# Kernel optimization log

Measured on AMD Instinct MI355X. Metric: run time of the kernel, lower is better.

## Reference

```python
import jax, jax.numpy as jnp
import numpy as np

K = 32        # neighbors per anchor (cfg.k)
LN_EPS = 1e-6 # flax LayerNorm default


def _layer_norm(x, g, b):
    mu = jnp.mean(x, axis=-1, keepdims=True)
    var = jnp.var(x, axis=-1, keepdims=True)
    return (x - mu) * jax.lax.rsqrt(var + LN_EPS) * g + b


def setup_inputs() -> dict:
    key = jax.random.key(0)
    ks = jax.random.split(key, 8)
    b, n, m, c = 4, 8192, 2048, 64
    feats, hidden = 128, 64  # cfg.features, cfg.features // 2
    cin = 3 + c              # delta_coord (3) concat neighbor feats (c)
    feat = jax.random.normal(ks[0], (b, n, c), jnp.float32)
    coord = jax.random.uniform(ks[1], (b, n, 3), jnp.float32)
    anchor_feat = jax.random.normal(ks[2], (b, m, c), jnp.float32)
    anchor_coord = jax.random.uniform(ks[3], (b, m, 3), jnp.float32)
    W1 = jax.random.normal(ks[4], (cin, hidden), jnp.float32) / np.sqrt(cin).astype(np.float32)
    b1 = jnp.zeros((hidden,), jnp.float32)
    g1 = jnp.ones((hidden,), jnp.float32)
    be1 = jnp.zeros((hidden,), jnp.float32)
    W2 = jax.random.normal(ks[5], (hidden, feats), jnp.float32) / np.sqrt(hidden).astype(np.float32)
    b2 = jnp.zeros((feats,), jnp.float32)
    g2 = jnp.ones((feats,), jnp.float32)
    be2 = jnp.zeros((feats,), jnp.float32)
    return dict(feat=feat, coord=coord, anchor_feat=anchor_feat,
                anchor_coord=anchor_coord, W1=W1, b1=b1, g1=g1, be1=be1,
                W2=W2, b2=b2, g2=g2, be2=be2)


def reference(feat, coord, anchor_feat, anchor_coord,
              W1, b1, g1, be1, W2, b2, g2, be2):
    # --- kNN: squared distances [b, m, n], take K smallest ---
    d2 = (jnp.sum(anchor_coord ** 2, axis=-1)[..., None]
          - 2.0 * jnp.einsum('bmd,bnd->bmn', anchor_coord, coord)
          + jnp.sum(coord ** 2, axis=-1)[:, None, :])
    _, idx = jax.lax.top_k(-d2, K)  # idx: [b, m, K]

    gather = jax.vmap(lambda arr, i: arr[i])  # batch_lookup
    k_feat = gather(feat, idx) - anchor_feat[..., None, :]   # [b,m,K,c] (anchor_feat_offset)
    k_coord = gather(coord, idx)                             # [b,m,K,3]

    delta = k_coord - anchor_coord[..., None, :]             # [b,m,K,3]
    norms = jnp.linalg.norm(delta, axis=-1, keepdims=True)   # [b,m,K,1]
    delta = delta / jnp.max(norms, axis=(-1, -2, -3), keepdims=True)  # per-batch max norm

    x = jnp.concatenate([delta, k_feat], axis=-1)            # [b,m,K,3+c]
    # GroupMLP: Dense -> LN -> relu, Dense -> LN -> relu, max pool over K
    x = jax.nn.relu(_layer_norm(x @ W1 + b1, g1, be1))
    x = jax.nn.relu(_layer_norm(x @ W2 + b2, g2, be2))
    return jnp.max(x, axis=-2)                               # [b, m, features]
```

## Files before the change

kernel.cpp:

```cpp
#include <hip/hip_runtime.h>
#include <math.h>

#define BB 4
#define NN 8192
#define MM 2048
#define CC 64
#define KNB 32
#define CIN 67
#define H1 64
#define H2 128
#define XP 36
#define AB 4
#define KT 512
#define PJ 16

__global__ void init_kernel(int* maxnorm) {
    if (threadIdx.x < BB) maxnorm[threadIdx.x] = 0;
}

__global__ __launch_bounds__(256) void coord4_kernel(const float* __restrict__ coord,
                                                     float4* __restrict__ c4) {
    const int t = blockIdx.x * 256 + threadIdx.x;
    if (t < BB * NN) {
        float cx = coord[t * 3 + 0], cy = coord[t * 3 + 1], cz = coord[t * 3 + 2];
        float c2 = __fadd_rn(__fadd_rn(__fmul_rn(cx, cx), __fmul_rn(cy, cy)), __fmul_rn(cz, cz));
        float4 q; q.x = cx; q.y = cy; q.z = cz; q.w = c2;
        c4[t] = q;
    }
}

__global__ __launch_bounds__(KT, 8) void knn_kernel(
    const float4* __restrict__ c4buf, const float* __restrict__ anchor_coord,
    int* __restrict__ idxbuf, int* __restrict__ maxnorm)
{
    __shared__ unsigned hist[2][4][256];
    __shared__ unsigned wmax[2][8];
    __shared__ unsigned wtot[2][4];
    __shared__ unsigned bc[2][2];
    __shared__ unsigned nsel[2];
    __shared__ int      selcell[2];
    __shared__ int      sel_s[2][KNB];

    const int a0 = blockIdx.x * 2;
    const int b  = a0 >> 11;
    const int mi = a0 & (MM - 1);
    const int tid = threadIdx.x;
    const int w = tid >> 6, lane = tid & 63;

    const float axA = anchor_coord[(b * MM + mi) * 3 + 0];
    const float ayA = anchor_coord[(b * MM + mi) * 3 + 1];
    const float azA = anchor_coord[(b * MM + mi) * 3 + 2];
    const float a2A = __fadd_rn(__fadd_rn(__fmul_rn(axA, axA), __fmul_rn(ayA, ayA)), __fmul_rn(azA, azA));
    const float axB = anchor_coord[(b * MM + mi + 1) * 3 + 0];
    const float ayB = anchor_coord[(b * MM + mi + 1) * 3 + 1];
    const float azB = anchor_coord[(b * MM + mi + 1) * 3 + 2];
    const float a2B = __fadd_rn(__fadd_rn(__fmul_rn(axB, axB), __fmul_rn(ayB, ayB)), __fmul_rn(azB, azB));

    const float4* c4b = c4buf + (size_t)b * NN;

    unsigned kregA[PJ], kregB[PJ];
    unsigned tminA = 0xFFFFFFFFu, tminB = 0xFFFFFFFFu;
    #pragma unroll
    for (int j = 0; j < PJ; j++) {
        const int i = tid + KT * j;
        const float4 cq = c4b[i];
        float dtA = __fadd_rn(__fadd_rn(__fmul_rn(axA, cq.x), __fmul_rn(ayA, cq.y)), __fmul_rn(azA, cq.z));
        float d2A = __fadd_rn(__fsub_rn(a2A, __fmul_rn(2.0f, dtA)), cq.w);
        unsigned ubA = __float_as_uint(d2A);
        ubA ^= (unsigned)((int)ubA >> 31) | 0x80000000u;
        kregA[j] = ubA;
        tminA = tminA < ubA ? tminA : ubA;
        float dtB = __fadd_rn(__fadd_rn(__fmul_rn(axB, cq.x), __fmul_rn(ayB, cq.y)), __fmul_rn(azB, cq.z));
        float d2B = __fadd_rn(__fsub_rn(a2B, __fmul_rn(2.0f, dtB)), cq.w);
        unsigned ubB = __float_as_uint(d2B);
        ubB ^= (unsigned)((int)ubB >> 31) | 0x80000000u;
        kregB[j] = ubB;
        tminB = tminB < ubB ? tminB : ubB;
    }

    unsigned umA = tminA, umB = tminB;
    umA = max(umA, (unsigned)__shfl_xor((int)umA, 1));
    umA = max(umA, (unsigned)__shfl_xor((int)umA, 2));
    umB = max(umB, (unsigned)__shfl_xor((int)umB, 1));
    umB = max(umB, (unsigned)__shfl_xor((int)umB, 2));
    if (lane == 0) { wmax[0][w] = umA; wmax[1][w] = umB; }
    if (tid == 0) { nsel[0] = 0; nsel[1] = 0; }
    __syncthreads();
    unsigned UA = wmax[0][0], UB = wmax[1][0];
    #pragma unroll
    for (int q = 1; q < 8; q++) { UA = max(UA, wmax[0][q]); UB = max(UB, wmax[1][q]); }

    unsigned prefA = 0, prefB = 0, pmask = 0;
    unsigned kA = KNB, kB = KNB;
    const int hc = w >> 1;

    #pragma unroll
    for (int pass = 0; pass < 4; pass++) {
        const int sh = 24 - 8 * pass;
        unsigned* hf = &hist[0][0][0];
        #pragma unroll
        for (int q = 0; q < 4; q++) hf[tid + KT * q] = 0;
        __syncthreads();
        if (pass == 0) {
            #pragma unroll
            for (int j = 0; j < PJ; j++) {
                if (kregA[j] <= UA) atomicAdd(&hist[0][hc][kregA[j] >> 24], 1u);
                if (kregB[j] <= UB) atomicAdd(&hist[1][hc][kregB[j] >> 24], 1u);
            }
        } else {
            #pragma unroll
            for (int j = 0; j < PJ; j++) {
                if ((kregA[j] & pmask) == prefA) atomicAdd(&hist[0][hc][(kregA[j] >> sh) & 0xFFu], 1u);
                if ((kregB[j] & pmask) == prefB) atomicAdd(&hist[1][hc][(kregB[j] >> sh) & 0xFFu], 1u);
            }
        }
        __syncthreads();
        if (tid < 256) {
            const unsigned hA = hist[0][0][tid] + hist[0][1][tid] + hist[0][2][tid] + hist[0][3][tid];
            const unsigned hB = hist[1][0][tid] + hist[1][1][tid] + hist[1][2][tid] + hist[1][3][tid];
            unsigned vA = hA, vB = hB;
            #pragma unroll
            for (int d = 1; d < 64; d <<= 1) {
                unsigned tA = __shfl_up(vA, d);
                unsigned tB = __shfl_up(vB, d);
                if (lane >= d) { vA += tA; vB += tB; }
            }
            if (lane == 63) { wtot[0][w] = vA; wtot[1][w] = vB; }
        }
        __syncthreads();
        if (tid < 256) {
            const unsigned hA = hist[0][0][tid] + hist[0][1][tid] + hist[0][2][tid] + hist[0][3][tid];
            const unsigned hB = hist[1][0][tid] + hist[1][1][tid] + hist[1][2][tid] + hist[1][3][tid];
            unsigned vA = hA, vB = hB;
            #pragma unroll
            for (int d = 1; d < 64; d <<= 1) {
                unsigned tA = __shfl_up(vA, d);
                unsigned tB = __shfl_up(vB, d);
                if (lane >= d) { vA += tA; vB += tB; }
            }
            unsigned offA = 0, offB = 0;
            #pragma unroll
            for (int ww = 0; ww < 3; ww++) if (ww < w) { offA += wtot[0][ww]; offB += wtot[1][ww]; }
            vA += offA; vB += offB;
            const unsigned exclA = vA - hA, exclB = vB - hB;
            if (exclA < kA && kA <= vA) { bc[0][0] = (unsigned)tid; bc[0][1] = kA - exclA; }
            if (exclB < kB && kB <= vB) { bc[1][0] = (unsigned)tid; bc[1][1] = kB - exclB; }
        }
        __syncthreads();
        prefA |= bc[0][0] << sh; kA = bc[0][1];
        prefB |= bc[1][0] << sh; kB = bc[1][1];
        pmask |= 0xFFu << sh;
    }
    const unsigned TA = prefA, TB = prefB;

    unsigned tiemaskA = 0, tiemaskB = 0;
    #pragma unroll
    for (int j = 0; j < PJ; j++) {
        unsigned kkA = kregA[j];
        if (kkA < TA) { unsigned p = atomicAdd(&nsel[0], 1u); sel_s[0][p] = tid + KT * j; }
        else if (kkA == TA) tiemaskA |= 1u << j;
        unsigned kkB = kregB[j];
        if (kkB < TB) { unsigned p = atomicAdd(&nsel[1], 1u); sel_s[1][p] = tid + KT * j; }
        else if (kkB == TB) tiemaskB |= 1u << j;
    }
    __syncthreads();
    {
        const unsigned n_lt = nsel[0];
        const unsigned needed = KNB - n_lt;
        int last = -1;
        for (unsigned r = 0; r < needed; r++) {
            if (tid == 0) selcell[0] = 0x7fffffff;
            __syncthreads();
            unsigned m = tiemaskA;
            while (m) {
                int j = __ffs(m) - 1; m &= m - 1;
                int idx = tid + KT * j;
                if (idx > last) atomicMin(&selcell[0], idx);
            }
            __syncthreads();
            last = selcell[0];
            if (tid == 0) sel_s[0][n_lt + r] = last;
            __syncthreads();
        }
    }
    {
        const unsigned n_lt = nsel[1];
        const unsigned needed = KNB - n_lt;
        int last = -1;
        for (unsigned r = 0; r < needed; r++) {
            if (tid == 0) selcell[1] = 0x7fffffff;
            __syncthreads();
            unsigned m = tiemaskB;
            while (m) {
                int j = __ffs(m) - 1; m &= m - 1;
                int idx = tid + KT * j;
                if (idx > last) atomicMin(&selcell[1], idx);
            }
            __syncthreads();
            last = selcell[1];
            if (tid == 0) sel_s[1][n_lt + r] = last;
            __syncthreads();
        }
    }

    float nrm = 0.0f;
    if (tid < 64) {
        const int a = tid >> 5;
        const int s = tid & 31;
        const int j = sel_s[a][s];
        idxbuf[(size_t)(a0 + a) * KNB + s] = j;
        const float4 cq = c4b[j];
        const float ax = a ? axB : axA, ay = a ? ayB : ayA, az = a ? azB : azA;
        float dx = __fsub_rn(cq.x, ax);
        float dy = __fsub_rn(cq.y, ay);
        float dz = __fsub_rn(cq.z, az);
        nrm = sqrtf(dx * dx + dy * dy + dz * dz);
        #pragma unroll
        for (int off = 32; off; off >>= 1) nrm = fmaxf(nrm, __shfl_xor(nrm, off));
        if (tid == 0) atomicMax(&maxnorm[b], __float_as_int(nrm));
    }
}

__global__ __launch_bounds__(256, 4) void mlp_kernel(
    const float* __restrict__ feat, const float* __restrict__ coord,
    const float* __restrict__ anchor_feat, const float* __restrict__ anchor_coord,
    const float* __restrict__ W1, const float* __restrict__ b1,
    const float* __restrict__ g1, const float* __restrict__ be1,
    const float* __restrict__ W2, const float* __restrict__ b2,
    const float* __restrict__ g2, const float* __restrict__ be2,
    const int* __restrict__ maxnorm, const int* __restrict__ idxbuf,
    float* __restrict__ out)
{
    __shared__ __align__(16) float xst[AB][CIN * XP];
    __shared__ int sel[AB][KNB];

    const int a0g = blockIdx.x * AB;
    const int b   = a0g >> 11;
    const int tid = threadIdx.x;
    const int w = tid >> 6, lane = tid & 63;
    const int g = tid >> 5, c = tid & 31;

    if (tid < AB * KNB) sel[tid >> 5][tid & 31] = idxbuf[(size_t)a0g * KNB + tid];
    __syncthreads();

    const float mn = __int_as_float(maxnorm[b]);

    {
        const int mi = (a0g + w) & (MM - 1);
        const float af = anchor_feat[((size_t)b * MM + mi) * CC + lane];
        #pragma unroll 8
        for (int kk = 0; kk < KNB; kk++) {
            const int nj = sel[w][kk];
            xst[w][(3 + lane) * XP + kk] = feat[((size_t)b * NN + nj) * CC + lane] - af;
        }
    }
    for (int t = tid; t < AB * KNB * 3; t += 256) {
        const int a = t / 96, r = t % 96, k = r / 3, j = r % 3;
        const int mi = (a0g + a) & (MM - 1);
        const int nj = sel[a][k];
        float d = __fsub_rn(coord[((size_t)b * NN + nj) * 3 + j],
                            anchor_coord[((size_t)b * MM + mi) * 3 + j]);
        xst[a][j * XP + k] = __fdiv_rn(d, mn);
    }
    __syncthreads();

    const int ch1 = 2 * c;
    const float b1a = b1[ch1], b1b = b1[ch1 + 1];
    float accA[AB][4], accB[AB][4];
    #pragma unroll
    for (int a = 0; a < AB; a++)
        #pragma unroll
        for (int kk = 0; kk < 4; kk++) { accA[a][kk] = b1a; accB[a][kk] = b1b; }
    #pragma unroll 4
    for (int j = 0; j < CIN; j++) {
        const float2 wv = *(const float2*)&W1[j * H1 + ch1];
        #pragma unroll
        for (int a = 0; a < AB; a++) {
            const float4 xq = *(const float4*)&xst[a][j * XP + 4 * g];
            accA[a][0] = fmaf(xq.x, wv.x, accA[a][0]);  accB[a][0] = fmaf(xq.x, wv.y, accB[a][0]);
            accA[a][1] = fmaf(xq.y, wv.x, accA[a][1]);  accB[a][1] = fmaf(xq.y, wv.y, accB[a][1]);
            accA[a][2] = fmaf(xq.z, wv.x, accA[a][2]);  accB[a][2] = fmaf(xq.z, wv.y, accB[a][2]);
            accA[a][3] = fmaf(xq.w, wv.x, accA[a][3]);  accB[a][3] = fmaf(xq.w, wv.y, accB[a][3]);
        }
    }
    const float g1a = g1[ch1], g1b = g1[ch1 + 1];
    const float be1a = be1[ch1], be1b = be1[ch1 + 1];
    float y1A[AB][4], y1B[AB][4];
    #pragma unroll
    for (int a = 0; a < AB; a++) {
        #pragma unroll
        for (int kk = 0; kk < 4; kk++) {
            float s  = accA[a][kk] + accB[a][kk];
            float s2 = accA[a][kk] * accA[a][kk] + accB[a][kk] * accB[a][kk];
            #pragma unroll
            for (int off = 16; off; off >>= 1) { s += __shfl_xor(s, off); s2 += __shfl_xor(s2, off); }
            float mu  = s  * (1.0f / H1);
            float var = s2 * (1.0f / H1) - mu * mu;
            float r = rsqrtf(var + 1e-6f);
            y1A[a][kk] = fmaxf(fmaf((accA[a][kk] - mu) * r, g1a, be1a), 0.0f);
            y1B[a][kk] = fmaxf(fmaf((accB[a][kk] - mu) * r, g1b, be1b), 0.0f);
        }
    }
    __syncthreads();
    #pragma unroll
    for (int a = 0; a < AB; a++)
        #pragma unroll
        for (int kk = 0; kk < 4; kk++) {
            xst[a][ch1 * XP + 4 * g + kk]       = y1A[a][kk];
            xst[a][(ch1 + 1) * XP + 4 * g + kk] = y1B[a][kk];
        }
    __syncthreads();

    const int ch2 = 4 * c;
    const float4 b2v = *(const float4*)&b2[ch2];
    float a2c[AB][16];
    #pragma unroll
    for (int a = 0; a < AB; a++)
        #pragma unroll
        for (int kk = 0; kk < 4; kk++) {
            a2c[a][0 * 4 + kk] = b2v.x; a2c[a][1 * 4 + kk] = b2v.y;
            a2c[a][2 * 4 + kk] = b2v.z; a2c[a][3 * 4 + kk] = b2v.w;
        }
    #pragma unroll 2
    for (int j = 0; j < H1; j++) {
        const float4 wv = *(const float4*)&W2[j * H2 + ch2];
        #pragma unroll
        for (int a = 0; a < AB; a++) {
            const float4 hq = *(const float4*)&xst[a][j * XP + 4 * g];
            a2c[a][0]  = fmaf(hq.x, wv.x, a2c[a][0]);  a2c[a][1]  = fmaf(hq.y, wv.x, a2c[a][1]);
            a2c[a][2]  = fmaf(hq.z, wv.x, a2c[a][2]);  a2c[a][3]  = fmaf(hq.w, wv.x, a2c[a][3]);
            a2c[a][4]  = fmaf(hq.x, wv.y, a2c[a][4]);  a2c[a][5]  = fmaf(hq.y, wv.y, a2c[a][5]);
            a2c[a][6]  = fmaf(hq.z, wv.y, a2c[a][6]);  a2c[a][7]  = fmaf(hq.w, wv.y, a2c[a][7]);
            a2c[a][8]  = fmaf(hq.x, wv.z, a2c[a][8]);  a2c[a][9]  = fmaf(hq.y, wv.z, a2c[a][9]);
            a2c[a][10] = fmaf(hq.z, wv.z, a2c[a][10]); a2c[a][11] = fmaf(hq.w, wv.z, a2c[a][11]);
            a2c[a][12] = fmaf(hq.x, wv.w, a2c[a][12]); a2c[a][13] = fmaf(hq.y, wv.w, a2c[a][13]);
            a2c[a][14] = fmaf(hq.z, wv.w, a2c[a][14]); a2c[a][15] = fmaf(hq.w, wv.w, a2c[a][15]);
        }
    }
    const float4 g2v  = *(const float4*)&g2[ch2];
    const float4 be2v = *(const float4*)&be2[ch2];
    float mx[AB][4];
    #pragma unroll
    for (int a = 0; a < AB; a++) {
        mx[a][0] = -INFINITY; mx[a][1] = -INFINITY; mx[a][2] = -INFINITY; mx[a][3] = -INFINITY;
        #pragma unroll
        for (int kk = 0; kk < 4; kk++) {
            float v0 = a2c[a][kk], v1 = a2c[a][4 + kk], v2 = a2c[a][8 + kk], v3 = a2c[a][12 + kk];
            float s  = (v0 + v1) + (v2 + v3);
            float s2 = (v0 * v0 + v1 * v1) + (v2 * v2 + v3 * v3);
            #pragma unroll
            for (int off = 16; off; off >>= 1) { s += __shfl_xor(s, off); s2 += __shfl_xor(s2, off); }
            float mu  = s  * (1.0f / H2);
            float var = s2 * (1.0f / H2) - mu * mu;
            float r = rsqrtf(var + 1e-6f);
            mx[a][0] = fmaxf(mx[a][0], fmaxf(fmaf((v0 - mu) * r, g2v.x, be2v.x), 0.0f));
            mx[a][1] = fmaxf(mx[a][1], fmaxf(fmaf((v1 - mu) * r, g2v.y, be2v.y), 0.0f));
            mx[a][2] = fmaxf(mx[a][2], fmaxf(fmaf((v2 - mu) * r, g2v.z, be2v.z), 0.0f));
            mx[a][3] = fmaxf(mx[a][3], fmaxf(fmaf((v3 - mu) * r, g2v.w, be2v.w), 0.0f));
        }
    }
    __syncthreads();
    float* pmaxp = &xst[0][0];
    #pragma unroll
    for (int a = 0; a < AB; a++) {
        float4 q; q.x = mx[a][0]; q.y = mx[a][1]; q.z = mx[a][2]; q.w = mx[a][3];
        *(float4*)&pmaxp[(a * 8 + g) * H2 + ch2] = q;
    }
    __syncthreads();
    #pragma unroll
    for (int t = tid; t < AB * H2; t += 256) {
        const int a = t >> 7, ch = t & 127;
        float vv = pmaxp[(a * 8 + 0) * H2 + ch];
        #pragma unroll
        for (int gg = 1; gg < 8; gg++) vv = fmaxf(vv, pmaxp[(a * 8 + gg) * H2 + ch]);
        out[(size_t)(a0g + a) * H2 + ch] = vv;
    }
}

extern "C" void kernel_launch(void* const* d_in, const int* in_sizes, int n_in,
                              void* d_out, int out_size, void* d_ws, size_t ws_size,
                              hipStream_t stream) {
    const float* feat         = (const float*)d_in[0];
    const float* coord        = (const float*)d_in[1];
    const float* anchor_feat  = (const float*)d_in[2];
    const float* anchor_coord = (const float*)d_in[3];
    const float* W1  = (const float*)d_in[4];
    const float* b1  = (const float*)d_in[5];
    const float* g1  = (const float*)d_in[6];
    const float* be1 = (const float*)d_in[7];
    const float* W2  = (const float*)d_in[8];
    const float* b2  = (const float*)d_in[9];
    const float* g2  = (const float*)d_in[10];
    const float* be2 = (const float*)d_in[11];
    float* out = (float*)d_out;

    int*    maxn   = (int*)d_ws;
    int*    idxbuf = (int*)d_ws + 16;
    float4* c4buf  = (float4*)((int*)d_ws + 16 + BB * MM * KNB);

    init_kernel<<<1, 64, 0, stream>>>(maxn);
    coord4_kernel<<<(BB * NN + 255) / 256, 256, 0, stream>>>(coord, c4buf);
    knn_kernel<<<BB * MM / 2, KT, 0, stream>>>(c4buf, anchor_coord, idxbuf, maxn);
    mlp_kernel<<<BB * MM / AB, 256, 0, stream>>>(feat, coord, anchor_feat, anchor_coord,
                                                 W1, b1, g1, be1, W2, b2, g2, be2,
                                                 maxn, idxbuf, out);
}
```

Baseline: 215.9 us.

## Process four anchors per kNN block to amortize coordinate loads and scans

The kNN kernel now handles four anchors per 512-thread block instead of two. Each coordinate load and each radix-select pass is shared across more anchors, and the scan work is split so all 512 threads take part, each half covering two anchors. The cost is many more live registers (64 keys per thread), with launch bounds lowered from 8 to 4 blocks, so occupancy may drop. Histogram copies per anchor fall from 4 to 2, which raises LDS atomic contention.

```diff
diff --git a/kernel.cpp b/kernel.cpp
--- a/kernel.cpp
+++ b/kernel.cpp
@@ -13,6 +13,7 @@
 #define AB 4
 #define KT 512
 #define PJ 16
+#define KAB 4
 
 __global__ void init_kernel(int* maxnorm) {
     if (threadIdx.x < BB) maxnorm[threadIdx.x] = 0;
@@ -29,19 +30,19 @@
     }
 }
 
-__global__ __launch_bounds__(KT, 8) void knn_kernel(
+__global__ __launch_bounds__(KT, 4) void knn_kernel(
     const float4* __restrict__ c4buf, const float* __restrict__ anchor_coord,
     int* __restrict__ idxbuf, int* __restrict__ maxnorm)
 {
-    __shared__ unsigned hist[2][4][256];
-    __shared__ unsigned wmax[2][8];
-    __shared__ unsigned wtot[2][4];
-    __shared__ unsigned bc[2][2];
-    __shared__ unsigned nsel[2];
-    __shared__ int      selcell[2];
-    __shared__ int      sel_s[2][KNB];
-
-    const int a0 = blockIdx.x * 2;
+    __shared__ unsigned hist[KAB][2][256];
+    __shared__ unsigned wmax[KAB][8];
+    __shared__ unsigned wtot[KAB][4];
+    __shared__ unsigned bc[KAB][2];
+    __shared__ unsigned nsel[KAB];
+    __shared__ int      selcell[KAB];
+    __shared__ int      sel_s[KAB][KNB];
+
+    const int a0 = blockIdx.x * KAB;
     const int b  = a0 >> 11;
     const int mi = a0 & (MM - 1);
     const int tid = threadIdx.x;
@@ -55,11 +56,19 @@
     const float ayB = anchor_coord[(b * MM + mi + 1) * 3 + 1];
     const float azB = anchor_coord[(b * MM + mi + 1) * 3 + 2];
     const float a2B = __fadd_rn(__fadd_rn(__fmul_rn(axB, axB), __fmul_rn(ayB, ayB)), __fmul_rn(azB, azB));
+    const float axC = anchor_coord[(b * MM + mi + 2) * 3 + 0];
+    const float ayC = anchor_coord[(b * MM + mi + 2) * 3 + 1];
+    const float azC = anchor_coord[(b * MM + mi + 2) * 3 + 2];
+    const float a2C = __fadd_rn(__fadd_rn(__fmul_rn(axC, axC), __fmul_rn(ayC, ayC)), __fmul_rn(azC, azC));
+    const float axD = anchor_coord[(b * MM + mi + 3) * 3 + 0];
+    const float ayD = anchor_coord[(b * MM + mi + 3) * 3 + 1];
+    const float azD = anchor_coord[(b * MM + mi + 3) * 3 + 2];
+    const float a2D = __fadd_rn(__fadd_rn(__fmul_rn(axD, axD), __fmul_rn(ayD, ayD)), __fmul_rn(azD, azD));
 
     const float4* c4b = c4buf + (size_t)b * NN;
 
-    unsigned kregA[PJ], kregB[PJ];
-    unsigned tminA = 0xFFFFFFFFu, tminB = 0xFFFFFFFFu;
+    unsigned kregA[PJ], kregB[PJ], kregC[PJ], kregD[PJ];
+    unsigned tminA = 0xFFFFFFFFu, tminB = 0xFFFFFFFFu, tminC = 0xFFFFFFFFu, tminD = 0xFFFFFFFFu;
     #pragma unroll
     for (int j = 0; j < PJ; j++) {
         const int i = tid + KT * j;
@@ -68,31 +77,42 @@
         float d2A = __fadd_rn(__fsub_rn(a2A, __fmul_rn(2.0f, dtA)), cq.w);
         unsigned ubA = __float_as_uint(d2A);
         ubA ^= (unsigned)((int)ubA >> 31) | 0x80000000u;
-        kregA[j] = ubA;
-        tminA = tminA < ubA ? tminA : ubA;
+        kregA[j] = ubA; tminA = tminA < ubA ? tminA : ubA;
         float dtB = __fadd_rn(__fadd_rn(__fmul_rn(axB, cq.x), __fmul_rn(ayB, cq.y)), __fmul_rn(azB, cq.z));
         float d2B = __fadd_rn(__fsub_rn(a2B, __fmul_rn(2.0f, dtB)), cq.w);
         unsigned ubB = __float_as_uint(d2B);
         ubB ^= (unsigned)((int)ubB >> 31) | 0x80000000u;
-        kregB[j] = ubB;
-        tminB = tminB < ubB ? tminB : ubB;
-    }
-
-    unsigned umA = tminA, umB = tminB;
-    umA = max(umA, (unsigned)__shfl_xor((int)umA, 1));
-    umA = max(umA, (unsigned)__shfl_xor((int)umA, 2));
-    umB = max(umB, (unsigned)__shfl_xor((int)umB, 1));
-    umB = max(umB, (unsigned)__shfl_xor((int)umB, 2));
-    if (lane == 0) { wmax[0][w] = umA; wmax[1][w] = umB; }
-    if (tid == 0) { nsel[0] = 0; nsel[1] = 0; }
-    __syncthreads();
-    unsigned UA = wmax[0][0], UB = wmax[1][0];
-    #pragma unroll
-    for (int q = 1; q < 8; q++) { UA = max(UA, wmax[0][q]); UB = max(UB, wmax[1][q]); }
-
-    unsigned prefA = 0, prefB = 0, pmask = 0;
-    unsigned kA = KNB, kB = KNB;
-    const int hc = w >> 1;
+        kregB[j] = ubB; tminB = tminB < ubB ? tminB : ubB;
+        float dtC = __fadd_rn(__fadd_rn(__fmul_rn(axC, cq.x), __fmul_rn(ayC, cq.y)), __fmul_rn(azC, cq.z));
+        float d2C = __fadd_rn(__fsub_rn(a2C, __fmul_rn(2.0f, dtC)), cq.w);
+        unsigned ubC = __float_as_uint(d2C);
+        ubC ^= (unsigned)((int)ubC >> 31) | 0x80000000u;
+        kregC[j] = ubC; tminC = tminC < ubC ? tminC : ubC;
+        float dtD = __fadd_rn(__fadd_rn(__fmul_rn(axD, cq.x), __fmul_rn(ayD, cq.y)), __fmul_rn(azD, cq.z));
+        float d2D = __fadd_rn(__fsub_rn(a2D, __fmul_rn(2.0f, dtD)), cq.w);
+        unsigned ubD = __float_as_uint(d2D);
+        ubD ^= (unsigned)((int)ubD >> 31) | 0x80000000u;
+        kregD[j] = ubD; tminD = tminD < ubD ? tminD : ubD;
+    }
+
+    unsigned umA = tminA, umB = tminB, umC = tminC, umD = tminD;
+    umA = max(umA, (unsigned)__shfl_xor((int)umA, 1)); umA = max(umA, (unsigned)__shfl_xor((int)umA, 2));
+    umB = max(umB, (unsigned)__shfl_xor((int)umB, 1)); umB = max(umB, (unsigned)__shfl_xor((int)umB, 2));
+    umC = max(umC, (unsigned)__shfl_xor((int)umC, 1)); umC = max(umC, (unsigned)__shfl_xor((int)umC, 2));
+    umD = max(umD, (unsigned)__shfl_xor((int)umD, 1)); umD = max(umD, (unsigned)__shfl_xor((int)umD, 2));
+    if (lane == 0) { wmax[0][w] = umA; wmax[1][w] = umB; wmax[2][w] = umC; wmax[3][w] = umD; }
+    if (tid < KAB) nsel[tid] = 0;
+    __syncthreads();
+    unsigned UA = wmax[0][0], UB = wmax[1][0], UC = wmax[2][0], UD = wmax[3][0];
+    #pragma unroll
+    for (int q = 1; q < 8; q++) {
+        UA = max(UA, wmax[0][q]); UB = max(UB, wmax[1][q]);
+        UC = max(UC, wmax[2][q]); UD = max(UD, wmax[3][q]);
+    }
+
+    unsigned prefA = 0, prefB = 0, prefC = 0, prefD = 0, pmask = 0;
+    unsigned kA = KNB, kB = KNB, kC = KNB, kD = KNB;
+    const int hc = w >> 2;
 
     #pragma unroll
     for (int pass = 0; pass < 4; pass++) {
@@ -106,118 +126,104 @@
             for (int j = 0; j < PJ; j++) {
                 if (kregA[j] <= UA) atomicAdd(&hist[0][hc][kregA[j] >> 24], 1u);
                 if (kregB[j] <= UB) atomicAdd(&hist[1][hc][kregB[j] >> 24], 1u);
+                if (kregC[j] <= UC) atomicAdd(&hist[2][hc][kregC[j] >> 24], 1u);
+                if (kregD[j] <= UD) atomicAdd(&hist[3][hc][kregD[j] >> 24], 1u);
             }
         } else {
             #pragma unroll
             for (int j = 0; j < PJ; j++) {
                 if ((kregA[j] & pmask) == prefA) atomicAdd(&hist[0][hc][(kregA[j] >> sh) & 0xFFu], 1u);
                 if ((kregB[j] & pmask) == prefB) atomicAdd(&hist[1][hc][(kregB[j] >> sh) & 0xFFu], 1u);
+                if ((kregC[j] & pmask) == prefC) atomicAdd(&hist[2][hc][(kregC[j] >> sh) & 0xFFu], 1u);
+                if ((kregD[j] & pmask) == prefD) atomicAdd(&hist[3][hc][(kregD[j] >> sh) & 0xFFu], 1u);
             }
         }
         __syncthreads();
-        if (tid < 256) {
-            const unsigned hA = hist[0][0][tid] + hist[0][1][tid] + hist[0][2][tid] + hist[0][3][tid];
-            const unsigned hB = hist[1][0][tid] + hist[1][1][tid] + hist[1][2][tid] + hist[1][3][tid];
-            unsigned vA = hA, vB = hB;
+        const int aa = (tid < 256) ? 0 : 2;
+        const int bin = tid & 255;
+        const int wg = w & 3;
+        const unsigned h0 = hist[aa][0][bin] + hist[aa][1][bin];
+        const unsigned h1 = hist[aa + 1][0][bin] + hist[aa + 1][1][bin];
+        unsigned v0 = h0, v1 = h1;
+        #pragma unroll
+        for (int d = 1; d < 64; d <<= 1) {
+            unsigned t0 = __shfl_up(v0, d);
+            unsigned t1 = __shfl_up(v1, d);
+            if (lane >= d) { v0 += t0; v1 += t1; }
+        }
+        if (lane == 63) { wtot[aa][wg] = v0; wtot[aa + 1][wg] = v1; }
+        __syncthreads();
+        {
+            unsigned off0 = 0, off1 = 0;
             #pragma unroll
-            for (int d = 1; d < 64; d <<= 1) {
-                unsigned tA = __shfl_up(vA, d);
-                unsigned tB = __shfl_up(vB, d);
-                if (lane >= d) { vA += tA; vB += tB; }
-            }
-            if (lane == 63) { wtot[0][w] = vA; wtot[1][w] = vB; }
-        }
-        __syncthreads();
-        if (tid < 256) {
-            const unsigned hA = hist[0][0][tid] + hist[0][1][tid] + hist[0][2][tid] + hist[0][3][tid];
-            const unsigned hB = hist[1][0][tid] + hist[1][1][tid] + hist[1][2][tid] + hist[1][3][tid];
-            unsigned vA = hA, vB = hB;
-            #pragma unroll
-            for (int d = 1; d < 64; d <<= 1) {
-                unsigned tA = __shfl_up(vA, d);
-                unsigned tB = __shfl_up(vB, d);
-                if (lane >= d) { vA += tA; vB += tB; }
-            }
-            unsigned offA = 0, offB = 0;
-            #pragma unroll
-            for (int ww = 0; ww < 3; ww++) if (ww < w) { offA += wtot[0][ww]; offB += wtot[1][ww]; }
-            vA += offA; vB += offB;
-            const unsigned exclA = vA - hA, exclB = vB - hB;
-            if (exclA < kA && kA <= vA) { bc[0][0] = (unsigned)tid; bc[0][1] = kA - exclA; }
-            if (exclB < kB && kB <= vB) { bc[1][0] = (unsigned)tid; bc[1][1] = kB - exclB; }
+            for (int ww = 0; ww < 3; ww++) if (ww < wg) { off0 += wtot[aa][ww]; off1 += wtot[aa + 1][ww]; }
+            v0 += off0; v1 += off1;
+            const unsigned k0 = (aa == 0) ? kA : kC;
+            const unsigned k1 = (aa == 0) ? kB : kD;
+            const unsigned excl0 = v0 - h0, excl1 = v1 - h1;
+            if (excl0 < k0 && k0 <= v0) { bc[aa][0] = (unsigned)bin; bc[aa][1] = k0 - excl0; }
+            if (excl1 < k1 && k1 <= v1) { bc[aa + 1][0] = (unsigned)bin; bc[aa + 1][1] = k1 - excl1; }
         }
         __syncthreads();
         prefA |= bc[0][0] << sh; kA = bc[0][1];
         prefB |= bc[1][0] << sh; kB = bc[1][1];
+        prefC |= bc[2][0] << sh; kC = bc[2][1];
+        prefD |= bc[3][0] << sh; kD = bc[3][1];
         pmask |= 0xFFu << sh;
     }
-    const unsigned TA = prefA, TB = prefB;
-
-    unsigned tiemaskA = 0, tiemaskB = 0;
+    const unsigned TA = prefA, TB = prefB, TC = prefC, TD = prefD;
+
+    unsigned tmA = 0, tmB = 0, tmC = 0, tmD = 0;
     #pragma unroll
     for (int j = 0; j < PJ; j++) {
-        unsigned kkA = kregA[j];
-        if (kkA < TA) { unsigned p = atomicAdd(&nsel[0], 1u); sel_s[0][p] = tid + KT * j; }
-        else if (kkA == TA) tiemaskA |= 1u << j;
-        unsigned kkB = kregB[j];
-        if (kkB < TB) { unsigned p = atomicAdd(&nsel[1], 1u); sel_s[1][p] = tid + KT * j; }
-        else if (kkB == TB) tiemaskB |= 1u << j;
-    }
-    __syncthreads();
-    {
-        const unsigned n_lt = nsel[0];
+        if (kregA[j] < TA) { unsigned p = atomicAdd(&nsel[0], 1u); sel_s[0][p] = tid + KT * j; }
+        else if (kregA[j] == TA) tmA |= 1u << j;
+        if (kregB[j] < TB) { unsigned p = atomicAdd(&nsel[1], 1u); sel_s[1][p] = tid + KT * j; }
+        else if (kregB[j] == TB) tmB |= 1u << j;
+        if (kregC[j] < TC) { unsigned p = atomicAdd(&nsel[2], 1u); sel_s[2][p] = tid + KT * j; }
+        else if (kregC[j] == TC) tmC |= 1u << j;
+        if (kregD[j] < TD) { unsigned p = atomicAdd(&nsel[3], 1u); sel_s[3][p] = tid + KT * j; }
+        else if (kregD[j] == TD) tmD |= 1u << j;
+    }
+    __syncthreads();
+    #pragma unroll
+    for (int a = 0; a < KAB; a++) {
+        const unsigned tmask = (a == 0) ? tmA : (a == 1) ? tmB : (a == 2) ? tmC : tmD;
+        const unsigned n_lt = nsel[a];
         const unsigned needed = KNB - n_lt;
         int last = -1;
         for (unsigned r = 0; r < needed; r++) {
-            if (tid == 0) selcell[0] = 0x7fffffff;
+            if (tid == 0) selcell[a] = 0x7fffffff;
             __syncthreads();
-            unsigned m = tiemaskA;
+            unsigned m = tmask;
             while (m) {
                 int j = __ffs(m) - 1; m &= m - 1;
                 int idx = tid + KT * j;
-                if (idx > last) atomicMin(&selcell[0], idx);
+                if (idx > last) atomicMin(&selcell[a], idx);
             }
             __syncthreads();
-            last = selcell[0];
-            if (tid == 0) sel_s[0][n_lt + r] = last;
+            last = selcell[a];
+            if (tid == 0) sel_s[a][n_lt + r] = last;
             __syncthreads();
         }
     }
-    {
-        const unsigned n_lt = nsel[1];
-        const unsigned needed = KNB - n_lt;
-        int last = -1;
-        for (unsigned r = 0; r < needed; r++) {
-            if (tid == 0) selcell[1] = 0x7fffffff;
-            __syncthreads();
-            unsigned m = tiemaskB;
-            while (m) {
-                int j = __ffs(m) - 1; m &= m - 1;
-                int idx = tid + KT * j;
-                if (idx > last) atomicMin(&selcell[1], idx);
-            }
-            __syncthreads();
-            last = selcell[1];
-            if (tid == 0) sel_s[1][n_lt + r] = last;
-            __syncthreads();
-        }
-    }
-
-    float nrm = 0.0f;
-    if (tid < 64) {
+
+    if (tid < 128) {
         const int a = tid >> 5;
         const int s = tid & 31;
         const int j = sel_s[a][s];
         idxbuf[(size_t)(a0 + a) * KNB + s] = j;
         const float4 cq = c4b[j];
-        const float ax = a ? axB : axA, ay = a ? ayB : ayA, az = a ? azB : azA;
+        const float ax = (a == 0) ? axA : (a == 1) ? axB : (a == 2) ? axC : axD;
+        const float ay = (a == 0) ? ayA : (a == 1) ? ayB : (a == 2) ? ayC : ayD;
+        const float az = (a == 0) ? azA : (a == 1) ? azB : (a == 2) ? azC : azD;
         float dx = __fsub_rn(cq.x, ax);
         float dy = __fsub_rn(cq.y, ay);
         float dz = __fsub_rn(cq.z, az);
-        nrm = sqrtf(dx * dx + dy * dy + dz * dz);
+        float nrm = sqrtf(dx * dx + dy * dy + dz * dz);
         #pragma unroll
         for (int off = 32; off; off >>= 1) nrm = fmaxf(nrm, __shfl_xor(nrm, off));
-        if (tid == 0) atomicMax(&maxnorm[b], __float_as_int(nrm));
+        if (lane == 0) atomicMax(&maxnorm[b], __float_as_int(nrm));
     }
 }
 
@@ -400,7 +406,7 @@
 
     init_kernel<<<1, 64, 0, stream>>>(maxn);
     coord4_kernel<<<(BB * NN + 255) / 256, 256, 0, stream>>>(coord, c4buf);
-    knn_kernel<<<BB * MM / 2, KT, 0, stream>>>(c4buf, anchor_coord, idxbuf, maxn);
+    knn_kernel<<<BB * MM / KAB, KT, 0, stream>>>(c4buf, anchor_coord, idxbuf, maxn);
     mlp_kernel<<<BB * MM / AB, 256, 0, stream>>>(feat, coord, anchor_feat, anchor_coord,
                                                  W1, b1, g1, be1, W2, b2, g2, be2,
                                                  maxn, idxbuf, out);
```

Result: no change. 218.7 us (+1.3%).
